# Performance work log

Hardware: AMD Instinct MI355X
Metric: run time of the kernel (lower is better)

## Reference

```python
import jax, jax.numpy as jnp
import numpy as np

V, E, H, D = 50257, 512, 512, 2  # vocab, embed_dim, hidden_dim, depth (nlayers)
B, S, T = 32, 60, 48             # batch, encoder len, target len


def setup_inputs() -> dict:
    key = jax.random.key(0)
    ks = jax.random.split(key, 9)
    return {
        "enc_h": jax.random.normal(ks[0], (B, S, 2 * H), jnp.float32),
        "prev_s": jax.random.normal(ks[1], (B, H), jnp.float32),
        "target": jax.random.randint(ks[2], (T, B), 0, V),
        "embed_W": jax.random.normal(ks[3], (V, E), jnp.float32) * 0.02,
        "attn_W": jax.random.normal(ks[4], (2 * H, H), jnp.float32) * (1.0 / np.sqrt(2 * H)),
        "attn_b": jnp.zeros((H,), jnp.float32),
        "inp_W": jax.random.normal(ks[5], (E, 2 * H), jnp.float32) * (1.0 / np.sqrt(E)),
        "inp_b": jnp.zeros((2 * H,), jnp.float32),
        "cell_W": jax.random.normal(ks[6], (D, H, 2 * H), jnp.float32) * (1.0 / np.sqrt(H)),
        "cell_b": jnp.zeros((D, 2 * H), jnp.float32),
        "out_W": jax.random.normal(ks[7], (H, V), jnp.float32) * (1.0 / np.sqrt(H)),
        "out_b": jnp.zeros((V,), jnp.float32),
    }


def reference(enc_h, prev_s, target, embed_W, attn_W, attn_b,
              inp_W, inp_b, cell_W, cell_b, out_W, out_b):
    # target: T x B -> embeddings T x B x E
    emb = embed_W[target]
    # enc_h is fixed across timesteps: precompute attention keys (B x S x H)
    energy = jnp.tanh(enc_h @ attn_W + attn_b)
    depth = cell_W.shape[0]

    def step(s, x_t):
        # attention: scores B x S, ctx B x 2H
        scores = jnp.einsum("bsh,bh->bs", energy, s)
        alpha = jax.nn.softmax(scores, axis=-1)
        ctx = jnp.einsum("bs,bsd->bd", alpha, enc_h)
        ctx_e = ctx[:, :E]  # module uses ctx[:, 0:embed_dim] (j never updated)
        for l in range(depth):  # small fixed depth loop
            Ws = (s * ctx_e) @ cell_W[l] + cell_b[l]
            if l == 0:
                Ws = Ws + x_t @ inp_W + inp_b
            hh, tt = jnp.split(Ws, 2, axis=1)
            hh = jnp.tanh(hh)
            tt = jax.nn.sigmoid(tt)
            s = hh * tt + s * (1.0 - tt)  # highway gate (dropout p=0)
        return s, s

    _, dec_h = jax.lax.scan(step, prev_s, emb)  # T x B x H
    return dec_h @ out_W + out_b  # T x B x V
```

## Files before the change

### kernel.cpp

```cpp
#include <hip/hip_runtime.h>
#include <hip/hip_bf16.h>
#include <math.h>

#define B_ 32
#define S_ 60
#define T_ 48
#define H_ 512
#define E_ 512
#define V_ 50257
#define NPAD 50432
#define EPI_LD 260
#define NTILE ((NPAD / 256) * 12)

typedef __attribute__((ext_vector_type(8))) short bf16x8v;
typedef __attribute__((ext_vector_type(4))) float f32x4v;
typedef __attribute__((ext_vector_type(4))) float f32x4a __attribute__((aligned(4)));
typedef __attribute__((ext_vector_type(4))) unsigned int u32x4;

__device__ inline unsigned short f2bf(float f) {
    union { float f; unsigned u; } v; v.f = f;
    unsigned r = v.u + 0x7fffu + ((v.u >> 16) & 1u);
    return (unsigned short)(r >> 16);
}
__device__ inline float bflo(unsigned u) { return __uint_as_float(u << 16); }

__device__ inline void gload_lds16(const void* g, void* l) {
    __builtin_amdgcn_global_load_lds(
        (const __attribute__((address_space(1))) unsigned int*)g,
        (__attribute__((address_space(3))) unsigned int*)l, 16, 0, 0);
}

__device__ __forceinline__ float ld_coh_f32_nw(const float* p) {
    float r;
    asm volatile("global_load_dword %0, %1, off sc0 sc1"
                 : "=v"(r) : "v"(p) : "memory");
    return r;
}
__device__ __forceinline__ void st_coh_f32(float* p, float v) {
    asm volatile("global_store_dword %0, %1, off sc0 sc1"
                 :: "v"(p), "v"(v) : "memory");
}
__device__ __forceinline__ void st_coh_u16(unsigned short* p, unsigned int v) {
    asm volatile("global_store_short %0, %1, off sc0 sc1"
                 :: "v"(p), "v"(v) : "memory");
}
__device__ __forceinline__ void st_coh_u32(int* p, int v) {
    asm volatile("global_store_dword %0, %1, off sc0 sc1"
                 :: "v"(p), "v"(v) : "memory");
}
__device__ __forceinline__ void st_coh_u64(unsigned long long* p, unsigned long long v) {
    asm volatile("global_store_dwordx2 %0, %1, off sc0 sc1"
                 :: "v"(p), "v"(v) : "memory");
}
__device__ __forceinline__ int ld_coh_u32(const int* p) {
    int r;
    asm volatile("global_load_dword %0, %1, off sc0 sc1\n\ts_waitcnt vmcnt(0)"
                 : "=v"(r) : "v"(p) : "memory");
    return r;
}
__device__ __forceinline__ u32x4 ld_cohx4(const void* p) {
    u32x4 r;
    asm volatile("global_load_dwordx4 %0, %1, off sc0 sc1"
                 : "=v"(r) : "v"(p) : "memory");
    return r;
}

__device__ __forceinline__ void gbar(int* flags, int idx, int bi) {
    asm volatile("s_waitcnt vmcnt(0)" ::: "memory");
    __syncthreads();
    if (threadIdx.x == 0)
        st_coh_u32(&flags[idx * 32 + bi], 1);
    if (threadIdx.x < 64) {
        const int* fp = &flags[idx * 32 + (threadIdx.x & 31)];
        for (;;) {
            int v = ld_coh_u32(fp);
            if (__all(v != 0)) break;
            __builtin_amdgcn_s_sleep(1);
        }
    }
    __syncthreads();
}

template<int ACT, bool GATHER, int MR>
__device__ void gemm_body(const float* __restrict__ A, const float* __restrict__ Bm,
                          const float* __restrict__ bias, float* __restrict__ C,
                          int N, int K, int lda, const int* __restrict__ gidx,
                          int cb, int rb, float (*As)[128], float (*Bs)[128])
{
    const int tid = threadIdx.x;
    const int am = (MR == 128) ? (tid >> 1) : ((tid & 127) >> 1);
    const int ak = (tid & 1) * 4;
    const bool aact = (MR == 128) || (tid < 128);
    const int arow = rb + am;
    const float* Arow;
    if (GATHER) Arow = A + (size_t)gidx[arow] * lda;
    else        Arow = A + (size_t)arow * lda;

    const int bk = tid >> 5;
    const int bn = (tid & 31) * 4;

    const int tx = tid & 15, ty = tid >> 4;
    float acc[MR / 16][8];
    #pragma unroll
    for (int i = 0; i < MR / 16; i++)
        #pragma unroll
        for (int j = 0; j < 8; j++) acc[i][j] = 0.f;

    for (int k0 = 0; k0 < K; k0 += 8) {
        float4 av, bv;
        if (aact) av = *(const float4*)(Arow + k0 + ak);
        bv = *(const float4*)(Bm + (size_t)(k0 + bk) * N + cb + bn);
        __syncthreads();
        if (aact) {
            As[ak + 0][am] = av.x; As[ak + 1][am] = av.y;
            As[ak + 2][am] = av.z; As[ak + 3][am] = av.w;
        }
        Bs[bk][bn + 0] = bv.x; Bs[bk][bn + 1] = bv.y;
        Bs[bk][bn + 2] = bv.z; Bs[bk][bn + 3] = bv.w;
        __syncthreads();

        #pragma unroll
        for (int k = 0; k < 8; k++) {
            float a[MR / 16], b[8];
            if constexpr (MR == 128) {
                *(float4*)(a)     = *(const float4*)&As[k][ty * 4];
                *(float4*)(a + 4) = *(const float4*)&As[k][ty * 4 + 64];
            } else {
                *(float4*)(a)     = *(const float4*)&As[k][ty * 4];
            }
            *(float4*)(b)     = *(const float4*)&Bs[k][tx * 4];
            *(float4*)(b + 4) = *(const float4*)&Bs[k][tx * 4 + 64];
            #pragma unroll
            for (int i = 0; i < MR / 16; i++)
                #pragma unroll
                for (int j = 0; j < 8; j++)
                    acc[i][j] = fmaf(a[i], b[j], acc[i][j]);
        }
    }

    #pragma unroll
    for (int i = 0; i < MR / 16; i++) {
        int row;
        if constexpr (MR == 128)
            row = rb + ((i < 4) ? (ty * 4 + i) : (64 + ty * 4 + (i - 4)));
        else
            row = rb + ty * 4 + i;
        #pragma unroll
        for (int j = 0; j < 8; j++) {
            int col = cb + ((j < 4) ? (tx * 4 + j) : (64 + tx * 4 + (j - 4)));
            float v = acc[i][j] + bias[col];
            if (ACT == 1) v = tanhf(v);
            C[(size_t)row * N + col] = v;
        }
    }
}

__global__ __launch_bounds__(256)
void gemm_pro(const float* __restrict__ enc_h, const float* __restrict__ attn_W,
              const float* __restrict__ attn_b, float* __restrict__ energy,
              const float* __restrict__ embed_W, const float* __restrict__ inp_W,
              const float* __restrict__ inp_b, float* __restrict__ pre,
              const int* __restrict__ target, int* __restrict__ cnt)
{
    __shared__ float As[8][128];
    __shared__ float Bs[8][128];
    const int bx = blockIdx.x;
    if (bx < 120) {
        const int cb = (bx & 3) * 128, rb = (bx >> 2) * 64;
        gemm_body<1, false, 64>(enc_h, attn_W, attn_b, energy,
                                512, 1024, 1024, nullptr, cb, rb, As, Bs);
    } else if (bx < 216) {
        const int b2 = bx - 120;
        const int cb = (b2 & 7) * 128, rb = (b2 >> 3) * 128;
        gemm_body<0, true, 128>(embed_W, inp_W, inp_b, pre,
                                1024, 512, 512, target, cb, rb, As, Bs);
    } else {
        for (int i = threadIdx.x; i < 144 * 32; i += 256)
            st_coh_u32(&cnt[i], 0);
    }
}

union __align__(16) ScanSM {
    struct {
        float eL[S_][H_];
        float part[8 * 32 * 36];
        float sCol[512];
    } s;
    float til[2 * 32 * 33];
    char g[49152];
};

template<int LI>
__device__ __forceinline__ void highway(
    int t, int bi, int tid, int lane, int wv,
    const bf16x8v (&wf)[2][2],
    const unsigned short* __restrict__ xsrc,
    unsigned short* __restrict__ xG1,
    const float* __restrict__ ctxG,
    float* __restrict__ sG,
    unsigned short* __restrict__ dec_b,
    const float* __restrict__ pre,
    float cbh, float cbt,
    float* part, float* sCol)
{
    const int l15 = lane & 15, lc = lane >> 4;
    const int b = tid >> 4, hi = tid & 15;
    const int h = bi * 16 + hi;

    float cxv = 0.f, prh = 0.f, prt = 0.f;
    if (LI == 0) {
        cxv = ld_coh_f32_nw(ctxG + (size_t)b * 512 + h);
        const float* pr = pre + ((size_t)t * B_ + b) * 1024;
        prh = pr[h]; prt = pr[h + 512];
    }

    u32x4 xr[2][2][2];
    #pragma unroll
    for (int ktl = 0; ktl < 2; ++ktl)
        #pragma unroll
        for (int pl = 0; pl < 2; ++pl)
            #pragma unroll
            for (int mt = 0; mt < 2; ++mt) {
                int ch = (((wv * 2 + ktl) * 2 + pl) * 4 + lc) * 32 + mt * 16 + l15;
                xr[ktl][pl][mt] = ld_cohx4(xsrc + (size_t)ch * 8);
            }
    asm volatile("s_waitcnt vmcnt(0)" ::: "memory");
    __builtin_amdgcn_sched_barrier(0);

    f32x4v acc[2][2];
    #pragma unroll
    for (int mt = 0; mt < 2; ++mt)
        #pragma unroll
        for (int nt = 0; nt < 2; ++nt) acc[mt][nt] = (f32x4v)0.f;

    #pragma unroll
    for (int ktl = 0; ktl < 2; ++ktl)
        #pragma unroll
        for (int pl = 0; pl < 2; ++pl)
            #pragma unroll
            for (int mt = 0; mt < 2; ++mt) {
                bf16x8v xv = *(bf16x8v*)&xr[ktl][pl][mt];
                #pragma unroll
                for (int nt = 0; nt < 2; ++nt)
                    acc[mt][nt] = __builtin_amdgcn_mfma_f32_16x16x32_bf16(
                        wf[ktl][nt], xv, acc[mt][nt], 0, 0, 0);
            }

    #pragma unroll
    for (int mt = 0; mt < 2; ++mt)
        #pragma unroll
        for (int nt = 0; nt < 2; ++nt)
            *(f32x4v*)&part[(wv * 32 + mt * 16 + l15) * 36 + nt * 16 + lc * 4] = acc[mt][nt];
    __syncthreads();

    float rh = 0.f, rt = 0.f;
    #pragma unroll
    for (int w = 0; w < 8; ++w) {
        rh += part[(w * 32 + b) * 36 + hi];
        rt += part[(w * 32 + b) * 36 + 16 + hi];
    }
    float ph = rh + cbh, pt = rt + cbt;
    if (LI == 0) { ph += prh; pt += prt; }
    float hh = tanhf(ph);
    float tg = 1.f / (1.f + __expf(-pt));
    float sold = sCol[tid];
    float sn = hh * tg + sold * (1.f - tg);
    sCol[tid] = sn;
    if (LI == 0) {
        float x1 = sn * cxv;
        unsigned short xh = f2bf(x1);
        unsigned short xl = f2bf(x1 - bflo((unsigned)xh));
        int kt = h >> 5, lc2 = (h >> 3) & 3, jj = h & 7;
        int ch = (kt * 8 + lc2) * 32 + b;
        st_coh_u16(xG1 + (size_t)ch * 8 + jj, xh);
        st_coh_u16(xG1 + (size_t)(ch + 128) * 8 + jj, xl);
    } else {
        st_coh_f32(sG + ((size_t)bi * 32 + b) * 16 + hi, sn);
        st_coh_u16(dec_b + ((size_t)bi * 1536 + (size_t)t * B_ + b) * 16 + hi,
                   f2bf(sn));
    }
}

__global__ __launch_bounds__(512, 2)
void scan_tr(const float* __restrict__ energy, const float* __restrict__ enc_h,
             const float* __restrict__ prev_s, const float* __restrict__ pre,
             const float* __restrict__ cell_W, const float* __restrict__ cell_b,
             unsigned short* __restrict__ dec_b,
             const float* __restrict__ outW, unsigned short* __restrict__ Wt,
             float* __restrict__ ctxG, float* __restrict__ sG,
             unsigned short* __restrict__ xG0, unsigned short* __restrict__ xG1,
             int* __restrict__ cnt,
             const float* __restrict__ out_b, float* __restrict__ out)
{
    __shared__ ScanSM sm;
    const int tid = threadIdx.x;
    int* aggF = cnt + 108 * 32;

    if (blockIdx.x >= B_) {
        const int hb = blockIdx.x - B_;
        const int g = tid >> 8;
        const int tt0 = tid & 255;
        const int r = tt0 >> 3, c4 = (tt0 & 7) * 4;
        float* til = sm.til;
        #pragma unroll 1
        for (int j = 0; j < 57; ++j) {
            const int tt = hb * 2 + g + j * 448;
            const bool act = tt < (NPAD / 32) * 16;
            int n0 = 0, k0 = 0;
            if (act) {
                n0 = (tt >> 4) * 32;
                k0 = (tt & 15) * 32;
                #pragma unroll
                for (int jj = 0; jj < 4; ++jj) {
                    int n = n0 + c4 + jj;
                    til[(g * 32 + r) * 33 + c4 + jj] =
                        (n < V_) ? __builtin_nontemporal_load(&outW[(size_t)(k0 + r) * V_ + n]) : 0.f;
                }
            }
            __syncthreads();
            if (act) {
                const int n = n0 + r;
                unsigned lo = (unsigned)f2bf(til[(g * 32 + c4 + 0) * 33 + r])
                            | ((unsigned)f2bf(til[(g * 32 + c4 + 1) * 33 + r]) << 16);
                unsigned hi2 = (unsigned)f2bf(til[(g * 32 + c4 + 2) * 33 + r])
                             | ((unsigned)f2bf(til[(g * 32 + c4 + 3) * 33 + r]) << 16);
                unsigned long long ov = (unsigned long long)lo | ((unsigned long long)hi2 << 32);
                st_coh_u64((unsigned long long*)&Wt[(size_t)n * 512 + k0 + c4], ov);
            }
            __syncthreads();
        }

        {
            int* hF = cnt + 101 * 32;
            asm volatile("s_waitcnt vmcnt(0)" ::: "memory");
            __syncthreads();
            if (tid == 0) st_coh_u32(&hF[hb], 1);
            if (tid < 64) {
                for (;;) {
                    int ok = 1;
                    #pragma unroll
                    for (int q = 0; q < 4; ++q) {
                        int idx = (tid & 63) + q * 64;
                        int v = (idx < 224) ? ld_coh_u32(&hF[idx]) : 1;
                        ok &= (v != 0);
                    }
                    if (__all(ok)) break;
                    __builtin_amdgcn_s_sleep(16);
                }
            }
            __syncthreads();
        }

        {
            short* As_wt  = (short*)sm.g;
            short* Bs_dec = (short*)(sm.g + 32768);
            float* epi    = (float*)sm.g;
            const int lane = tid & 63, w = tid >> 6;
            const int wm = w >> 2, wn = w & 3;

#define STAGE_TILE(bix, kt, rb, cb) do {                                      \
            short* Ab_ = As_wt + (bix) * 8192;                                \
            short* Bb_ = Bs_dec + (bix) * 4096;                               \
            _Pragma("unroll")                                                 \
            for (int j_ = 0; j_ < 2; ++j_) {                                  \
                int rg_ = w * 2 + j_;                                         \
                int row_ = rg_ * 16 + (lane >> 2);                            \
                int kc_ = (lane & 3) ^ (row_ & 3);                            \
                gload_lds16(Wt + ((size_t)((cb) + row_) * 512 + (kt) * 32 + kc_ * 8), \
                            Ab_ + rg_ * 512);                                 \
            }                                                                 \
            {                                                                 \
                int row_ = w * 16 + (lane >> 2);                              \
                int kc_ = (lane & 3) ^ (row_ & 3);                            \
                gload_lds16(dec_b + (((size_t)((kt) * 2 + (kc_ >> 1)) * 1536 + ((rb) + row_)) * 16 \
                                     + (kc_ & 1) * 8),                        \
                            Bb_ + w * 512);                                   \
            }                                                                 \
        } while (0)

            #pragma unroll 1
            for (int i = hb; i < NTILE; i += 224) {
                const int rbi = i / 197;
                const int rb  = rbi * 128;
                const int cb  = (i % 197) * 256;
                const int need = rbi * 4 + 4;

                if (tid < 64) {
                    for (;;) {
                        int v = ld_coh_u32(aggF);
                        if (__all(v >= need)) break;
                        __builtin_amdgcn_s_sleep(16);
                    }
                }
                __syncthreads();

                f32x4v acc[4][4];
                #pragma unroll
                for (int mi = 0; mi < 4; ++mi)
                    #pragma unroll
                    for (int ni = 0; ni < 4; ++ni) acc[mi][ni] = (f32x4v)0.f;

                STAGE_TILE(0, 0, rb, cb);

                #pragma unroll 1
                for (int it = 0; it < 16; ++it) {
                    const int cur = it & 1;
                    __builtin_amdgcn_s_barrier();
                    asm volatile("" ::: "memory");
                    if (it < 15) {
                        STAGE_TILE(cur ^ 1, it + 1, rb, cb);
                        asm volatile("s_waitcnt vmcnt(3)" ::: "memory");
                    } else {
                        asm volatile("s_waitcnt vmcnt(0)" ::: "memory");
                    }
                    __builtin_amdgcn_s_barrier();
                    asm volatile("" ::: "memory");

                    const short* Ab = As_wt + cur * 8192;
                    const short* Bb = Bs_dec + cur * 4096;
                    bf16x8v af[4], bf[4];
                    const int lc = lane >> 4;
                    #pragma unroll
                    for (int ni = 0; ni < 4; ++ni) {
                        int r_ = wn * 64 + ni * 16 + (lane & 15);
                        af[ni] = *(const bf16x8v*)&Ab[r_ * 32 + ((lc ^ (r_ & 3)) * 8)];
                    }
                    #pragma unroll
                    for (int mi = 0; mi < 4; ++mi) {
                        int r_ = wm * 64 + mi * 16 + (lane & 15);
                        bf[mi] = *(const bf16x8v*)&Bb[r_ * 32 + ((lc ^ (r_ & 3)) * 8)];
                    }
                    #pragma unroll
                    for (int mi = 0; mi < 4; ++mi)
                        #pragma unroll
                        for (int ni = 0; ni < 4; ++ni)
                            acc[mi][ni] = __builtin_amdgcn_mfma_f32_16x16x32_bf16(
                                af[ni], bf[mi], acc[mi][ni], 0, 0, 0);
                }

                const int c4e = (tid & 63) * 4;
                const bool fullcols = (cb + 256 <= V_);
                f32x4v bq = (f32x4v)0.f;
                if (fullcols) {
                    float4 t4 = *(const float4*)(out_b + cb + c4e);
                    bq[0] = t4.x; bq[1] = t4.y; bq[2] = t4.z; bq[3] = t4.w;
                }
                #pragma unroll
                for (int mi = 0; mi < 4; ++mi) {
                    __syncthreads();
                    #pragma unroll
                    for (int ni = 0; ni < 4; ++ni) {
                        const int er = wm * 16 + (lane & 15);
                        const int ec = wn * 64 + ni * 16 + (lane >> 4) * 4;
                        *(f32x4v*)&epi[er * EPI_LD + ec] = acc[mi][ni];
                    }
                    __syncthreads();
                    #pragma unroll
                    for (int j = 0; j < 4; ++j) {
                        const int rr = w + j * 8;
                        const int orow = rb + (rr >> 4) * 64 + mi * 16 + (rr & 15);
                        f32x4v v = *(const f32x4v*)&epi[rr * EPI_LD + c4e];
                        if (fullcols) {
                            v += bq;
                            *(f32x4a*)(out + (size_t)orow * V_ + cb + c4e) = v;
                        } else {
                            #pragma unroll
                            for (int vv = 0; vv < 4; ++vv) {
                                const int col = cb + c4e + vv;
                                if (col < V_)
                                    out[(size_t)orow * V_ + col] = v[vv] + out_b[col];
                            }
                        }
                    }
                }
            }
#undef STAGE_TILE
        }
        return;
    }

    const int bi = blockIdx.x;
    const int lane = tid & 63, wv = tid >> 6;
    float (*eL)[H_] = sm.s.eL;
    float* part   = sm.s.part;
    float* sA     = part;
    float* scoreL = part + 512;
    float* alphaL = part + 576;
    float* sCol   = sm.s.sCol;
    int*   sF     = cnt + 100 * 32;

    for (int i = tid; i < S_ * H_ / 4; i += 512) {
        int s = i >> 7, h4 = (i & 127) * 4;
        *(float4*)&eL[s][h4] = *(const float4*)&energy[((size_t)bi * S_ + s) * 512 + h4];
    }

    bf16x8v wf0[2][2], wf1[2][2];
    {
        const int l15 = lane & 15, lc = lane >> 4;
        #pragma unroll
        for (int ktl = 0; ktl < 2; ++ktl)
            #pragma unroll
            for (int nt = 0; nt < 2; ++nt) {
                const int kb = (wv * 2 + ktl) * 32 + lc * 8;
                const int n  = nt * 512 + bi * 16 + l15;
                #pragma unroll
                for (int jj = 0; jj < 8; ++jj) {
                    wf0[ktl][nt][jj] = (short)f2bf(cell_W[((size_t)(kb + jj)) * 1024 + n]);
                    wf1[ktl][nt][jj] = (short)f2bf(cell_W[((size_t)(512 + kb + jj)) * 1024 + n]);
                }
            }
    }
    const int hME = bi * 16 + (tid & 15);
    sCol[tid] = prev_s[(size_t)(tid >> 4) * 512 + hME];
    const float cb0h = cell_b[hME],        cb0t = cell_b[512 + hME];
    const float cb1h = cell_b[1024 + hME], cb1t = cell_b[1536 + hME];

    #pragma unroll 1
    for (int t = 0; t < T_; ++t) {
        float sAv;
        if (t == 0) {
            sAv = prev_s[(size_t)bi * 512 + tid];
            __syncthreads();
            sA[tid] = sAv;
            __syncthreads();
        } else {
            const int* fp = &sF[tid >> 4];
            for (;;) {
                int v = ld_coh_u32(fp);
                if (v >= t) break;
                __builtin_amdgcn_s_sleep(1);
            }
            sAv = ld_coh_f32_nw(sG + ((size_t)(tid >> 4) * 32 + bi) * 16 + (tid & 15));
            __syncthreads();
            asm volatile("s_waitcnt vmcnt(0)" ::: "memory");
            sA[tid] = sAv;
            __syncthreads();
            if (bi == 0 && tid == 0)
                st_coh_u32(aggF, t);
        }

        #pragma unroll 1
        for (int sp = 0; sp < 4; ++sp) {
            const int s0 = wv + sp * 16;
            const int s1 = s0 + 8;
            const bool has1 = (sp < 3) | (wv < 4);
            const float* e0 = &eL[s0][lane];
            const float* e1 = &eL[has1 ? s1 : s0][lane];
            float a0 = 0.f, a1 = 0.f;
            #pragma unroll
            for (int j = 0; j < 8; ++j) {
                float sv = sA[lane + j * 64];
                a0 = fmaf(e0[j * 64], sv, a0);
                a1 = fmaf(e1[j * 64], sv, a1);
            }
            #pragma unroll
            for (int off = 32; off; off >>= 1) {
                a0 += __shfl_xor(a0, off, 64);
                a1 += __shfl_xor(a1, off, 64);
            }
            if (lane == 0) {
                scoreL[s0] = a0;
                if (has1) scoreL[s1] = a1;
            }
        }
        __syncthreads();
        if (wv == 0) {
            float v = (lane < S_) ? scoreL[lane] : -3.4e38f;
            float m = v;
            #pragma unroll
            for (int off = 32; off; off >>= 1) m = fmaxf(m, __shfl_xor(m, off, 64));
            float e = (lane < S_) ? __expf(v - m) : 0.f;
            float su = e;
            #pragma unroll
            for (int off = 32; off; off >>= 1) su += __shfl_xor(su, off, 64);
            if (lane < S_) alphaL[lane] = e / su;
        }
        __syncthreads();
        {
            float a = 0.f;
            const float* ep = enc_h + (size_t)bi * S_ * 1024 + tid;
            #pragma unroll 20
            for (int s = 0; s < S_; ++s) a = fmaf(alphaL[s], ep[(size_t)s * 1024], a);
            st_coh_f32(ctxG + (size_t)bi * 512 + tid, a);
            float x0 = a * sA[tid];
            unsigned short xh = f2bf(x0);
            unsigned short xl = f2bf(x0 - bflo((unsigned)xh));
            int kt = tid >> 5, lc2 = (tid >> 3) & 3, jj = tid & 7;
            int ch = (kt * 8 + lc2) * 32 + bi;
            st_coh_u16(xG0 + (size_t)ch * 8 + jj, xh);
            st_coh_u16(xG0 + (size_t)(ch + 128) * 8 + jj, xl);
        }
        gbar(cnt, 2 * t + 0, bi);
        highway<0>(t, bi, tid, lane, wv, wf0, xG0, xG1, ctxG, sG, dec_b, pre,
                   cb0h, cb0t, part, sCol);
        gbar(cnt, 2 * t + 1, bi);
        highway<1>(t, bi, tid, lane, wv, wf1, xG1, xG1, ctxG, sG, dec_b, pre,
                   cb1h, cb1t, part, sCol);
        asm volatile("s_waitcnt vmcnt(0)" ::: "memory");
        __syncthreads();
        if (tid == 0)
            st_coh_u32(&sF[bi], t + 1);
    }

    if (bi == 0) {
        if (tid < 64) {
            const int* fp2 = &sF[tid & 31];
            for (;;) {
                int v = ld_coh_u32(fp2);
                if (__all(v >= T_)) break;
                __builtin_amdgcn_s_sleep(1);
            }
        }
        __syncthreads();
        if (tid == 0)
            st_coh_u32(aggF, T_);
    }
}

extern "C" void kernel_launch(void* const* d_in, const int* in_sizes, int n_in,
                              void* d_out, int out_size, void* d_ws, size_t ws_size,
                              hipStream_t stream)
{
    const float* enc_h   = (const float*)d_in[0];
    const float* prev_s  = (const float*)d_in[1];
    const int*   target  = (const int*)  d_in[2];
    const float* embed_W = (const float*)d_in[3];
    const float* attn_W  = (const float*)d_in[4];
    const float* attn_b  = (const float*)d_in[5];
    const float* inp_W   = (const float*)d_in[6];
    const float* inp_b   = (const float*)d_in[7];
    const float* cell_W  = (const float*)d_in[8];
    const float* cell_b  = (const float*)d_in[9];
    const float* out_W   = (const float*)d_in[10];
    const float* out_b   = (const float*)d_in[11];
    float* out = (float*)d_out;

    float* ws = (float*)d_ws;
    float* energy = ws;
    float* pre    = energy + (size_t)B_ * S_ * H_;
    float* ctxG   = pre + (size_t)T_ * B_ * 2 * H_;
    float* sG     = ctxG + (size_t)B_ * H_;
    int*   cnt    = (int*)(sG + (size_t)B_ * H_);
    unsigned short* dec_b = (unsigned short*)(cnt + 144 * 32);
    unsigned short* xG0   = dec_b + (size_t)T_ * B_ * H_;
    unsigned short* xG1   = xG0 + (size_t)2 * B_ * H_;
    unsigned short* Wt    = xG1 + (size_t)2 * B_ * H_;

    gemm_pro<<<217, 256, 0, stream>>>(enc_h, attn_W, attn_b, energy,
                                      embed_W, inp_W, inp_b, pre, target, cnt);

    scan_tr<<<256, 512, 0, stream>>>(energy, enc_h, prev_s, pre, cell_W, cell_b,
                                     dec_b, out_W, Wt, ctxG, sG, xG0, xG1, cnt,
                                     out_b, out);
}
```

Measured before the change: 789.8 us.

## Fold prologue GEMMs into scan kernel helper blocks with flag sync

Removes the separate prologue GEMM launch. The 224 helper blocks of the scan kernel now compute the energy and input-projection GEMMs in two 256-thread teams and signal per-block ready flags, which the 32 scan blocks wait on before loading energy. The flag reset moves to a hipMemsetAsync. The output-projection tiling also changes from a strided tile loop to one fixed column strip per helper block, iterating over row blocks. This aims to cut launch and tail overhead and overlap prologue work with weight conversion, at the cost of more spin-waiting and a less balanced split of the output GEMM.

```diff
diff --git a/kernel.cpp b/kernel.cpp
--- a/kernel.cpp
+++ b/kernel.cpp
@@ -10,7 +10,7 @@
 #define V_ 50257
 #define NPAD 50432
 #define EPI_LD 260
-#define NTILE ((NPAD / 256) * 12)
+#define NCOL (NPAD / 256)
 
 typedef __attribute__((ext_vector_type(8))) short bf16x8v;
 typedef __attribute__((ext_vector_type(4))) float f32x4v;
@@ -81,16 +81,16 @@
     __syncthreads();
 }
 
-template<int ACT, bool GATHER, int MR>
-__device__ void gemm_body(const float* __restrict__ A, const float* __restrict__ Bm,
+template<int ACT, bool GATHER>
+__device__ void gemm_team(int tid, const float* __restrict__ A,
+                          const float* __restrict__ Bm,
                           const float* __restrict__ bias, float* __restrict__ C,
                           int N, int K, int lda, const int* __restrict__ gidx,
                           int cb, int rb, float (*As)[128], float (*Bs)[128])
 {
-    const int tid = threadIdx.x;
-    const int am = (MR == 128) ? (tid >> 1) : ((tid & 127) >> 1);
+    const int am = (tid & 127) >> 1;
     const int ak = (tid & 1) * 4;
-    const bool aact = (MR == 128) || (tid < 128);
+    const bool aact = (tid < 128);
     const int arow = rb + am;
     const float* Arow;
     if (GATHER) Arow = A + (size_t)gidx[arow] * lda;
@@ -100,9 +100,9 @@
     const int bn = (tid & 31) * 4;
 
     const int tx = tid & 15, ty = tid >> 4;
-    float acc[MR / 16][8];
+    float acc[4][8];
     #pragma unroll
-    for (int i = 0; i < MR / 16; i++)
+    for (int i = 0; i < 4; i++)
         #pragma unroll
         for (int j = 0; j < 8; j++) acc[i][j] = 0.f;
 
@@ -121,17 +121,12 @@
 
         #pragma unroll
         for (int k = 0; k < 8; k++) {
-            float a[MR / 16], b[8];
-            if constexpr (MR == 128) {
-                *(float4*)(a)     = *(const float4*)&As[k][ty * 4];
-                *(float4*)(a + 4) = *(const float4*)&As[k][ty * 4 + 64];
-            } else {
-                *(float4*)(a)     = *(const float4*)&As[k][ty * 4];
-            }
+            float a[4], b[8];
+            *(float4*)(a)     = *(const float4*)&As[k][ty * 4];
             *(float4*)(b)     = *(const float4*)&Bs[k][tx * 4];
             *(float4*)(b + 4) = *(const float4*)&Bs[k][tx * 4 + 64];
             #pragma unroll
-            for (int i = 0; i < MR / 16; i++)
+            for (int i = 0; i < 4; i++)
                 #pragma unroll
                 for (int j = 0; j < 8; j++)
                     acc[i][j] = fmaf(a[i], b[j], acc[i][j]);
@@ -139,44 +134,15 @@
     }
 
     #pragma unroll
-    for (int i = 0; i < MR / 16; i++) {
-        int row;
-        if constexpr (MR == 128)
-            row = rb + ((i < 4) ? (ty * 4 + i) : (64 + ty * 4 + (i - 4)));
-        else
-            row = rb + ty * 4 + i;
+    for (int i = 0; i < 4; i++) {
+        int row = rb + ty * 4 + i;
         #pragma unroll
         for (int j = 0; j < 8; j++) {
             int col = cb + ((j < 4) ? (tx * 4 + j) : (64 + tx * 4 + (j - 4)));
             float v = acc[i][j] + bias[col];
             if (ACT == 1) v = tanhf(v);
-            C[(size_t)row * N + col] = v;
-        }
-    }
-}
-
-__global__ __launch_bounds__(256)
-void gemm_pro(const float* __restrict__ enc_h, const float* __restrict__ attn_W,
-              const float* __restrict__ attn_b, float* __restrict__ energy,
-              const float* __restrict__ embed_W, const float* __restrict__ inp_W,
-              const float* __restrict__ inp_b, float* __restrict__ pre,
-              const int* __restrict__ target, int* __restrict__ cnt)
-{
-    __shared__ float As[8][128];
-    __shared__ float Bs[8][128];
-    const int bx = blockIdx.x;
-    if (bx < 120) {
-        const int cb = (bx & 3) * 128, rb = (bx >> 2) * 64;
-        gemm_body<1, false, 64>(enc_h, attn_W, attn_b, energy,
-                                512, 1024, 1024, nullptr, cb, rb, As, Bs);
-    } else if (bx < 216) {
-        const int b2 = bx - 120;
-        const int cb = (b2 & 7) * 128, rb = (b2 >> 3) * 128;
-        gemm_body<0, true, 128>(embed_W, inp_W, inp_b, pre,
-                                1024, 512, 512, target, cb, rb, As, Bs);
-    } else {
-        for (int i = threadIdx.x; i < 144 * 32; i += 256)
-            st_coh_u32(&cnt[i], 0);
+            st_coh_f32(&C[(size_t)row * N + col], v);
+        }
     }
 }
 
@@ -186,6 +152,7 @@
         float part[8 * 32 * 36];
         float sCol[512];
     } s;
+    struct { float As[2][8][128]; float Bs[2][8][128]; } p;
     float til[2 * 32 * 33];
     char g[49152];
 };
@@ -282,8 +249,12 @@
 }
 
 __global__ __launch_bounds__(512, 2)
-void scan_tr(const float* __restrict__ energy, const float* __restrict__ enc_h,
-             const float* __restrict__ prev_s, const float* __restrict__ pre,
+void scan_tr(const float* __restrict__ enc_h, const float* __restrict__ attn_W,
+             const float* __restrict__ attn_b, float* __restrict__ energy,
+             const float* __restrict__ embed_W, const float* __restrict__ inp_W,
+             const float* __restrict__ inp_b, float* __restrict__ pre,
+             const int* __restrict__ target,
+             const float* __restrict__ prev_s,
              const float* __restrict__ cell_W, const float* __restrict__ cell_b,
              unsigned short* __restrict__ dec_b,
              const float* __restrict__ outW, unsigned short* __restrict__ Wt,
@@ -295,39 +266,64 @@
     __shared__ ScanSM sm;
     const int tid = threadIdx.x;
     int* aggF = cnt + 108 * 32;
+    int* pF   = cnt + 110 * 32;
 
     if (blockIdx.x >= B_) {
         const int hb = blockIdx.x - B_;
-        const int g = tid >> 8;
-        const int tt0 = tid & 255;
-        const int r = tt0 >> 3, c4 = (tt0 & 7) * 4;
-        float* til = sm.til;
-        #pragma unroll 1
-        for (int j = 0; j < 57; ++j) {
-            const int tt = hb * 2 + g + j * 448;
-            const bool act = tt < (NPAD / 32) * 16;
-            int n0 = 0, k0 = 0;
-            if (act) {
-                n0 = (tt >> 4) * 32;
-                k0 = (tt & 15) * 32;
-                #pragma unroll
-                for (int jj = 0; jj < 4; ++jj) {
-                    int n = n0 + c4 + jj;
-                    til[(g * 32 + r) * 33 + c4 + jj] =
-                        (n < V_) ? __builtin_nontemporal_load(&outW[(size_t)(k0 + r) * V_ + n]) : 0.f;
-                }
-            }
-            __syncthreads();
-            if (act) {
-                const int n = n0 + r;
-                unsigned lo = (unsigned)f2bf(til[(g * 32 + c4 + 0) * 33 + r])
-                            | ((unsigned)f2bf(til[(g * 32 + c4 + 1) * 33 + r]) << 16);
-                unsigned hi2 = (unsigned)f2bf(til[(g * 32 + c4 + 2) * 33 + r])
-                             | ((unsigned)f2bf(til[(g * 32 + c4 + 3) * 33 + r]) << 16);
-                unsigned long long ov = (unsigned long long)lo | ((unsigned long long)hi2 << 32);
-                st_coh_u64((unsigned long long*)&Wt[(size_t)n * 512 + k0 + c4], ov);
-            }
-            __syncthreads();
+
+        if (hb < 156) {
+            const int team = tid >> 8, t0 = tid & 255;
+            if (hb < 60) {
+                int e = hb * 2 + team;
+                gemm_team<1, false>(t0, enc_h, attn_W, attn_b, energy,
+                                    512, 1024, 1024, nullptr,
+                                    (e & 3) * 128, (e >> 2) * 64,
+                                    sm.p.As[team], sm.p.Bs[team]);
+            } else {
+                int p = (hb - 60) * 2 + team;
+                gemm_team<0, true>(t0, embed_W, inp_W, inp_b, pre,
+                                   1024, 512, 512, target,
+                                   (p & 7) * 128, (p >> 3) * 64,
+                                   sm.p.As[team], sm.p.Bs[team]);
+            }
+            asm volatile("s_waitcnt vmcnt(0)" ::: "memory");
+            __syncthreads();
+            if (tid == 0) st_coh_u32(&pF[hb], 1);
+            __syncthreads();
+        }
+
+        {
+            const int g = tid >> 8;
+            const int tt0 = tid & 255;
+            const int r = tt0 >> 3, c4 = (tt0 & 7) * 4;
+            float* til = sm.til;
+            #pragma unroll 1
+            for (int j = 0; j < 57; ++j) {
+                const int tt = hb * 2 + g + j * 448;
+                const bool act = tt < (NPAD / 32) * 16;
+                int n0 = 0, k0 = 0;
+                if (act) {
+                    n0 = (tt >> 4) * 32;
+                    k0 = (tt & 15) * 32;
+                    #pragma unroll
+                    for (int jj = 0; jj < 4; ++jj) {
+                        int n = n0 + c4 + jj;
+                        til[(g * 32 + r) * 33 + c4 + jj] =
+                            (n < V_) ? __builtin_nontemporal_load(&outW[(size_t)(k0 + r) * V_ + n]) : 0.f;
+                    }
+                }
+                __syncthreads();
+                if (act) {
+                    const int n = n0 + r;
+                    unsigned lo = (unsigned)f2bf(til[(g * 32 + c4 + 0) * 33 + r])
+                                | ((unsigned)f2bf(til[(g * 32 + c4 + 1) * 33 + r]) << 16);
+                    unsigned hi2 = (unsigned)f2bf(til[(g * 32 + c4 + 2) * 33 + r])
+                                 | ((unsigned)f2bf(til[(g * 32 + c4 + 3) * 33 + r]) << 16);
+                    unsigned long long ov = (unsigned long long)lo | ((unsigned long long)hi2 << 32);
+                    st_coh_u64((unsigned long long*)&Wt[(size_t)n * 512 + k0 + c4], ov);
+                }
+                __syncthreads();
+            }
         }
 
         {
@@ -351,14 +347,16 @@
             __syncthreads();
         }
 
-        {
+        const int ci = hb;
+        if (ci < NCOL) {
             short* As_wt  = (short*)sm.g;
             short* Bs_dec = (short*)(sm.g + 32768);
             float* epi    = (float*)sm.g;
             const int lane = tid & 63, w = tid >> 6;
             const int wm = w >> 2, wn = w & 3;
-
-#define STAGE_TILE(bix, kt, rb, cb) do {                                      \
+            const int cb = ci * 256;
+
+#define STAGE_TILE(bix, kt, rb) do {                                          \
             short* Ab_ = As_wt + (bix) * 8192;                                \
             short* Bb_ = Bs_dec + (bix) * 4096;                               \
             _Pragma("unroll")                                                 \
@@ -366,7 +364,7 @@
                 int rg_ = w * 2 + j_;                                         \
                 int row_ = rg_ * 16 + (lane >> 2);                            \
                 int kc_ = (lane & 3) ^ (row_ & 3);                            \
-                gload_lds16(Wt + ((size_t)((cb) + row_) * 512 + (kt) * 32 + kc_ * 8), \
+                gload_lds16(Wt + ((size_t)(cb + row_) * 512 + (kt) * 32 + kc_ * 8), \
                             Ab_ + rg_ * 512);                                 \
             }                                                                 \
             {                                                                 \
@@ -379,17 +377,15 @@
         } while (0)
 
             #pragma unroll 1
-            for (int i = hb; i < NTILE; i += 224) {
-                const int rbi = i / 197;
-                const int rb  = rbi * 128;
-                const int cb  = (i % 197) * 256;
+            for (int rbi = 0; rbi < 12; ++rbi) {
+                const int rb   = rbi * 128;
                 const int need = rbi * 4 + 4;
 
                 if (tid < 64) {
                     for (;;) {
                         int v = ld_coh_u32(aggF);
                         if (__all(v >= need)) break;
-                        __builtin_amdgcn_s_sleep(16);
+                        __builtin_amdgcn_s_sleep(32);
                     }
                 }
                 __syncthreads();
@@ -400,7 +396,7 @@
                     #pragma unroll
                     for (int ni = 0; ni < 4; ++ni) acc[mi][ni] = (f32x4v)0.f;
 
-                STAGE_TILE(0, 0, rb, cb);
+                STAGE_TILE(0, 0, rb);
 
                 #pragma unroll 1
                 for (int it = 0; it < 16; ++it) {
@@ -408,7 +404,7 @@
                     __builtin_amdgcn_s_barrier();
                     asm volatile("" ::: "memory");
                     if (it < 15) {
-                        STAGE_TILE(cur ^ 1, it + 1, rb, cb);
+                        STAGE_TILE(cur ^ 1, it + 1, rb);
                         asm volatile("s_waitcnt vmcnt(3)" ::: "memory");
                     } else {
                         asm volatile("s_waitcnt vmcnt(0)" ::: "memory");
@@ -489,11 +485,6 @@
     float* sCol   = sm.s.sCol;
     int*   sF     = cnt + 100 * 32;
 
-    for (int i = tid; i < S_ * H_ / 4; i += 512) {
-        int s = i >> 7, h4 = (i & 127) * 4;
-        *(float4*)&eL[s][h4] = *(const float4*)&energy[((size_t)bi * S_ + s) * 512 + h4];
-    }
-
     bf16x8v wf0[2][2], wf1[2][2];
     {
         const int l15 = lane & 15, lc = lane >> 4;
@@ -514,6 +505,26 @@
     sCol[tid] = prev_s[(size_t)(tid >> 4) * 512 + hME];
     const float cb0h = cell_b[hME],        cb0t = cell_b[512 + hME];
     const float cb1h = cell_b[1024 + hME], cb1t = cell_b[1536 + hME];
+
+    if (tid < 64) {
+        for (;;) {
+            int ok = 1;
+            #pragma unroll
+            for (int q = 0; q < 3; ++q) {
+                int idx = tid + q * 64;
+                int v = (idx < 156) ? ld_coh_u32(&pF[idx]) : 1;
+                ok &= (v != 0);
+            }
+            if (__all(ok)) break;
+            __builtin_amdgcn_s_sleep(8);
+        }
+    }
+    __syncthreads();
+
+    for (int i = tid; i < S_ * H_ / 4; i += 512) {
+        int s = i >> 7, h4 = (i & 127) * 4;
+        *(float4*)&eL[s][h4] = *(const float4*)&energy[((size_t)bi * S_ + s) * 512 + h4];
+    }
 
     #pragma unroll 1
     for (int t = 0; t < T_; ++t) {
@@ -646,10 +657,11 @@
     unsigned short* xG1   = xG0 + (size_t)2 * B_ * H_;
     unsigned short* Wt    = xG1 + (size_t)2 * B_ * H_;
 
-    gemm_pro<<<217, 256, 0, stream>>>(enc_h, attn_W, attn_b, energy,
-                                      embed_W, inp_W, inp_b, pre, target, cnt);
-
-    scan_tr<<<256, 512, 0, stream>>>(energy, enc_h, prev_s, pre, cell_W, cell_b,
+    hipMemsetAsync(cnt, 0, 144 * 32 * sizeof(int), stream);
+
+    scan_tr<<<256, 512, 0, stream>>>(enc_h, attn_W, attn_b, energy,
+                                     embed_W, inp_W, inp_b, pre, target,
+                                     prev_s, cell_W, cell_b,
                                      dec_b, out_W, Wt, ctxG, sG, xG0, xG1, cnt,
                                      out_b, out);
 }
```

Result: slower. 831.3 us (+5.3%).
